# Kernel optimization log

Hardware: AMD Instinct MI355X
Metric: run time of the kernel (lower is better)

## Reference

```python
import jax, jax.numpy as jnp
import numpy as np

IMG = 224      # img_size
P = 16         # patch_size
C = 3          # in_chans
K = 100        # n_segments
COMPACT = 10.0 # slic compactness
ITERS = 10     # slic k-means iterations


def _resize_matrix(src, dst):
    # Linear antialiased resize is a linear map; materialize it by resizing identity.
    return jax.image.resize(jnp.eye(src, dtype=jnp.float32), (dst, src),
                            method='linear', antialias=True)


def _slic_labels(img_hwc):
    """Simplified SLIC: grid-initialized k-means in (color, compactness-scaled xy) space."""
    H, W = IMG, IMG
    S = float(np.sqrt(H * W / K))         # superpixel spacing
    ratio = COMPACT / S                   # spatial scaling (SLIC distance weighting)
    yy, xx = jnp.meshgrid(jnp.arange(H, dtype=jnp.float32),
                          jnp.arange(W, dtype=jnp.float32), indexing='ij')
    feat = jnp.concatenate([img_hwc, (yy * ratio)[..., None], (xx * ratio)[..., None]],
                           axis=-1).reshape(H * W, C + 2)  # [HW, 5]
    # grid init of K centers
    gh = int(np.ceil(np.sqrt(K)))
    gw = int(np.ceil(K / gh))
    cy = ((np.arange(gh) + 0.5) * H / gh).astype(np.int32)
    cx = ((np.arange(gw) + 0.5) * W / gw).astype(np.int32)
    idx = (cy[:, None] * W + cx[None, :]).reshape(-1)[:K]
    centers0 = feat[jnp.asarray(idx)]  # [K, 5]

    f2 = jnp.sum(feat * feat, axis=1, keepdims=True)  # [HW,1]

    def dists(centers):
        c2 = jnp.sum(centers * centers, axis=1)  # [K]
        return f2 + c2[None, :] - 2.0 * (feat @ centers.T)  # [HW,K]

    def body(i, centers):
        lbl = jnp.argmin(dists(centers), axis=1)              # [HW]
        oh = jax.nn.one_hot(lbl, K, dtype=feat.dtype)         # [HW,K]
        cnt = oh.sum(0)                                       # [K]
        new = (oh.T @ feat) / jnp.maximum(cnt, 1.0)[:, None]  # [K,5]
        return jnp.where((cnt > 0)[:, None], new, centers)

    centers = jax.lax.fori_loop(0, ITERS, body, centers0)
    return jnp.argmin(dists(centers), axis=1).reshape(H, W)


def _embed_one(img_chw, A):
    img = jnp.transpose(img_chw, (1, 2, 0))                     # [H,W,C]
    labels = jax.lax.stop_gradient(_slic_labels(img))           # [H,W] int
    masks = jax.nn.one_hot(labels, K, dtype=img.dtype, axis=0)  # [K,H,W]
    masked = masks[..., None] * img[None]                       # [K,H,W,C]
    tmp = jnp.einsum('ph,khwc->kpwc', A, masked)                # resize rows
    return jnp.einsum('qw,kpwc->kpqc', A, tmp)                  # [K,P,P,C]


def reference(x):
    B = x.shape[0]
    A = _resize_matrix(IMG, P)
    sp = jax.vmap(lambda im: _embed_one(im, A))(x)  # [B,K,P,P,C]
    # torch: view(B, K*C, P, P)  (raw row-major reinterpret), flatten(2), transpose(1,2)
    out = sp.reshape(B, K * C, P, P).reshape(B, K * C, P * P)
    return jnp.transpose(out, (0, 2, 1))  # [B, P*P, K*C]


def setup_inputs() -> dict:
    key = jax.random.key(0)
    x = jax.random.uniform(key, (8, C, IMG, IMG), dtype=jnp.float32)
    return {"x": x}
```

## Files before the change

kernel.cpp:

```cpp
#include <hip/hip_runtime.h>
#include <math.h>

#define IMGD 224
#define HW 50176
#define NK 100
#define NB 8
#define OUT_PER_B 76800
#define NCHUNK 131
#define MSTR 13


static __device__ __forceinline__ float ratio_f32() {
  return (float)(10.0 / sqrt(224.0 * 224.0 / 100.0));
}

static __device__ __forceinline__ float dist5s(float f0, float f1, float f2,
                                               float f3, float f4, float fsq,
                                               float c0, float c1, float c2,
                                               float c3, float c4, float q) {
  float dot = __fmul_rn(f0, c0);
  dot = __fmaf_rn(f1, c1, dot);
  dot = __fmaf_rn(f2, c2, dot);
  dot = __fmaf_rn(f3, c3, dot);
  dot = __fmaf_rn(f4, c4, dot);
  return __fsub_rn(__fadd_rn(fsq, q), __fmul_rn(2.0f, dot));
}

static __device__ __forceinline__ float fsq5(float f0, float f1, float f2,
                                             float f3, float f4) {
  float s = __fmul_rn(f0, f0);
  s = __fadd_rn(s, __fmul_rn(f1, f1));
  s = __fadd_rn(s, __fmul_rn(f2, f2));
  s = __fadd_rn(s, __fmul_rn(f3, f3));
  s = __fadd_rn(s, __fmul_rn(f4, f4));
  return s;
}

__global__ void __launch_bounds__(256, 4) iter_kernel(
    const float* __restrict__ x, float* __restrict__ centers,
    const float* __restrict__ c2g, float* __restrict__ partials, int flag,
    float* __restrict__ Ag) {
  __shared__ float4 ck4[NK];
  __shared__ float2 ck2[NK];
  __shared__ unsigned int maskS[2][NK * MSTR];
  __shared__ unsigned short ppkS[2][NK * MSTR];
  __shared__ float4 cval4[2][384];
  __shared__ float  cvalf[2][384];
  __shared__ int cntS[2][128];
  __shared__ int offxS[2][128];
  __shared__ int wtotS[2];
  __shared__ float ubpart[2][12][10];
  __shared__ float ubg[2][12];
  __shared__ unsigned int candm[2][12][4];
  __shared__ float ared[128];
  int bx = blockIdx.x, b = blockIdx.y;
  int tid = threadIdx.x;

  if (bx >= 66) {
    for (int rr = 0; rr < 2; ++rr) {
      int p = 2 * b + rr;
      float cp = (p + 0.5f) * 14.0f - 0.5f;
      if (tid < 128) {
        float xd0 = fabsf(cp - (float)tid) / 14.0f;
        float trip0 = fmaxf(0.0f, 1.0f - xd0);
        float trip1 = 0.0f;
        int t2 = tid + 128;
        if (t2 < IMGD) {
          float xd = fabsf(cp - (float)t2) / 14.0f;
          trip1 = fmaxf(0.0f, 1.0f - xd);
        }
        ared[tid] = trip0 + trip1;
      }
      __syncthreads();
      for (int s = 64; s > 0; s >>= 1) {
        if (tid < s) ared[tid] += ared[tid + s];
        __syncthreads();
      }
      float Zp = ared[0];
      __syncthreads();
      if (tid < IMGD) {
        float xd = fabsf(cp - (float)tid) / 14.0f;
        Ag[p * IMGD + tid] = fmaxf(0.0f, 1.0f - xd) / Zp;
      }
      __syncthreads();
    }
    return;
  }

  int half = tid >> 7;
  int lt = tid & 127;
  int c = 2 * bx + half;
  int start, len;
  if (c < NCHUNK) {
    start = (c < 129) ? c * 384 : 49536 + (c - 129) * 320;
    len   = (c < 129) ? 384 : 320;
  } else {
    start = 0; len = 0;
  }

  const float ratio = ratio_f32();
  const float* x0 = x + (size_t)b * 3 * HW;
  if (flag == 0) {
    if (tid < NK) {
      int gy = tid / 10, gx = tid - 10 * (tid / 10);
      int cy = (int)((gy + 0.5) * 224.0 / 10.0);
      int cx = (int)((gx + 0.5) * 224.0 / 10.0);
      int i = cy * IMGD + cx;
      float c0 = x0[i], c1 = x0[HW + i], c2 = x0[2 * HW + i];
      float c3 = __fmul_rn((float)cy, ratio);
      float c4 = __fmul_rn((float)cx, ratio);
      float s = __fmul_rn(c0, c0);
      s = __fadd_rn(s, __fmul_rn(c1, c1));
      s = __fadd_rn(s, __fmul_rn(c2, c2));
      s = __fadd_rn(s, __fmul_rn(c3, c3));
      s = __fadd_rn(s, __fmul_rn(c4, c4));
      ck4[tid] = make_float4(c0, c1, c2, c3);
      ck2[tid] = make_float2(c4, s);
      if (bx == 0) {
        float* oc = centers + ((size_t)b * NK + tid) * 5;
        oc[0] = c0; oc[1] = c1; oc[2] = c2; oc[3] = c3; oc[4] = c4;
      }
    }
  } else {
    const float* cb = centers + (size_t)b * NK * 5;
    const float* c2b = c2g + (size_t)b * NK;
    if (tid < NK) {
      ck4[tid] = make_float4(cb[tid*5+0], cb[tid*5+1], cb[tid*5+2], cb[tid*5+3]);
      ck2[tid] = make_float2(cb[tid*5+4], c2b[tid]);
    }
  }
  for (int t = lt; t < NK * MSTR; t += 128) maskS[half][t] = 0u;
  if (lt < 48) candm[half][lt >> 2][lt & 3] = 0u;

  float f0[3], f1[3], f2[3], f3[3], f4[3], fq[3];
  bool vld[3];
  for (int r = 0; r < 3; ++r) {
    int t = lt + r * 128;
    vld[r] = (t < len);
    int i = start + (vld[r] ? t : 0);
    int y = i / IMGD, xw = i - y * IMGD;
    f0[r] = x0[i]; f1[r] = x0[HW + i]; f2[r] = x0[2 * HW + i];
    f3[r] = __fmul_rn((float)y, ratio);
    f4[r] = __fmul_rn((float)xw, ratio);
    fq[r] = fsq5(f0[r], f1[r], f2[r], f3[r], f4[r]);
  }
  __syncthreads();

  if (lt < 120) {
    int g = lt / 10, kb = lt - 10 * g;
    int i0 = start + g * 32, i1 = i0 + 31;
    int ymin = i0 / IMGD, ymax = i1 / IMGD;
    int cmin = (ymin == ymax) ? (i0 - ymin * IMGD) : 0;
    int cmax = (ymin == ymax) ? (i1 - ymax * IMGD) : (IMGD - 1);
    float f3mn = __fmul_rn((float)ymin, ratio);
    float f3mx = __fmul_rn((float)ymax, ratio);
    float f4mn = __fmul_rn((float)cmin, ratio);
    float f4mx = __fmul_rn((float)cmax, ratio);
    float mn = 3.4e38f;
    for (int k = kb * 10; k < kb * 10 + 10; ++k) {
      float c3 = ck4[k].w, c4 = ck2[k].x;
      float dy = fmaxf(fabsf(c3 - f3mn), fabsf(c3 - f3mx));
      float dx = fmaxf(fabsf(c4 - f4mn), fabsf(c4 - f4mx));
      mn = fminf(mn, dy * dy + dx * dx + 3.0f);
    }
    ubpart[half][g][kb] = mn;
  }
  __syncthreads();
  if (lt < 12) {
    float mn = ubpart[half][lt][0];
    for (int j = 1; j < 10; ++j) mn = fminf(mn, ubpart[half][lt][j]);
    ubg[half][lt] = mn + 1.0f;
  }
  __syncthreads();
  if (lt < 120) {
    int g = lt / 10, kb = lt - 10 * g;
    int i0 = start + g * 32, i1 = i0 + 31;
    int ymin = i0 / IMGD, ymax = i1 / IMGD;
    int cmin = (ymin == ymax) ? (i0 - ymin * IMGD) : 0;
    int cmax = (ymin == ymax) ? (i1 - ymax * IMGD) : (IMGD - 1);
    float f3mn = __fmul_rn((float)ymin, ratio);
    float f3mx = __fmul_rn((float)ymax, ratio);
    float f4mn = __fmul_rn((float)cmin, ratio);
    float f4mx = __fmul_rn((float)cmax, ratio);
    float lim = ubg[half][g];
    for (int k = kb * 10; k < kb * 10 + 10; ++k) {
      float c3 = ck4[k].w, c4 = ck2[k].x;
      float dy = fmaxf(0.0f, fmaxf(f3mn - c3, c3 - f3mx));
      float dx = fmaxf(0.0f, fmaxf(f4mn - c4, c4 - f4mx));
      if (dy * dy + dx * dx <= lim)
        atomicOr(&candm[half][g][k >> 5], 1u << (k & 31));
    }
  }
  __syncthreads();

  float best[3]; int bk[3];
  for (int r = 0; r < 3; ++r) {
    best[r] = 3.4e38f; bk[r] = 0;
    int t = lt + r * 128;
    int g = (t < 384) ? (t >> 5) : 0;
    for (int w = 0; w < 4; ++w) {
      unsigned int m = candm[half][g][w];
      while (m) {
        int j = __ffs(m) - 1;
        m &= m - 1;
        int k = (w << 5) + j;
        float4 a4 = ck4[k];
        float2 a2 = ck2[k];
        float d = dist5s(f0[r], f1[r], f2[r], f3[r], f4[r], fq[r],
                         a4.x, a4.y, a4.z, a4.w, a2.x, a2.y);
        if (d < best[r]) { best[r] = d; bk[r] = k; }
      }
    }
  }
  for (int r = 0; r < 3; ++r) {
    int t = lt + r * 128;
    if (vld[r]) atomicOr(&maskS[half][bk[r] * MSTR + (t >> 5)], 1u << (t & 31));
  }
  __syncthreads();

  int myCnt = 0;
  if (lt < NK) {
    int s = 0;
    for (int g = 0; g < 12; ++g) {
      ppkS[half][lt * MSTR + g] = (unsigned short)s;
      s += __popc(maskS[half][lt * MSTR + g]);
    }
    myCnt = s;
  }
  cntS[half][lt] = myCnt;
  __syncthreads();

  int v = myCnt;
  for (int d = 1; d < 64; d <<= 1) {
    int u = __shfl_up(v, d, 64);
    if ((tid & 63) >= d) v += u;
  }
  if (lt == 63) wtotS[half] = v;
  __syncthreads();
  if (lt >= 64) v += wtotS[half];
  offxS[half][lt] = v;
  __syncthreads();

  for (int r = 0; r < 3; ++r) {
    int t = lt + r * 128;
    if (vld[r]) {
      int g = t >> 5, j = t & 31;
      unsigned int m = maskS[half][bk[r] * MSTR + g];
      int rank = ppkS[half][bk[r] * MSTR + g] + __popc(m & ((1u << j) - 1u));
      int pos = offxS[half][bk[r]] - cntS[half][bk[r]] + rank;
      cval4[half][pos] = make_float4(f0[r], f1[r], f2[r], f3[r]);
      cvalf[half][pos] = f4[r];
    }
  }
  __syncthreads();

  if (c < NCHUNK && lt < NK) {
    int n = cntS[half][lt];
    int base = offxS[half][lt] - n;
    float s0 = 0.f, s1 = 0.f, s2 = 0.f, s3 = 0.f, s4 = 0.f, s5 = 0.f;
    for (int m = 0; m < n; ++m) {
      float4 vv = cval4[half][base + m];
      float ww = cvalf[half][base + m];
      s0 = __fadd_rn(s0, vv.x);
      s1 = __fadd_rn(s1, vv.y);
      s2 = __fadd_rn(s2, vv.z);
      s3 = __fadd_rn(s3, vv.w);
      s4 = __fadd_rn(s4, ww);
      s5 += 1.0f;
    }
    float* pp = partials + ((size_t)(b * NK + lt) * 6) * NCHUNK + c;
    pp[0 * NCHUNK] = s0; pp[1 * NCHUNK] = s1; pp[2 * NCHUNK] = s2;
    pp[3 * NCHUNK] = s3; pp[4 * NCHUNK] = s4; pp[5 * NCHUNK] = s5;
  }
}

__global__ void __launch_bounds__(256) combine_update_kernel(
    float* __restrict__ centers, const float* __restrict__ partials,
    float* __restrict__ c2g) {
  __shared__ float st[8 * 6 * NCHUNK];
  __shared__ float sums[8][6];
  __shared__ float newc[8][5];
  int bb = blockIdx.x;
  int tid = threadIdx.x;
  const float* base = partials + (size_t)bb * 8 * 6 * NCHUNK;
  for (int t = tid; t < (8 * 6 * NCHUNK) / 4; t += 256)
    ((float4*)st)[t] = ((const float4*)base)[t];
  __syncthreads();
  if (tid < 48) {
    int row = tid / 6, comp = tid - 6 * (tid / 6);
    const float* rp = st + (row * 6 + comp) * NCHUNK;
    float s = rp[0];
    for (int c = 1; c < NCHUNK; ++c) s = __fadd_rn(s, rp[c]);
    sums[row][comp] = s;
  }
  __syncthreads();
  if (tid < 40) {
    int row = tid / 5, d = tid - 5 * (tid / 5);
    float cntv = sums[row][5];
    float* cc = centers + (size_t)(bb * 8 + row) * 5;
    float v;
    if (cntv > 0.0f) {
      float m = fmaxf(cntv, 1.0f);
      v = __fdiv_rn(sums[row][d], m);
      cc[d] = v;
    } else {
      v = cc[d];
    }
    newc[row][d] = v;
  }
  __syncthreads();
  if (tid < 8) {
    float t0 = __fmul_rn(newc[tid][0], newc[tid][0]);
    t0 = __fadd_rn(t0, __fmul_rn(newc[tid][1], newc[tid][1]));
    t0 = __fadd_rn(t0, __fmul_rn(newc[tid][2], newc[tid][2]));
    t0 = __fadd_rn(t0, __fmul_rn(newc[tid][3], newc[tid][3]));
    t0 = __fadd_rn(t0, __fmul_rn(newc[tid][4], newc[tid][4]));
    c2g[bb * 8 + tid] = t0;
  }
}

__global__ void __launch_bounds__(128, 4) label_kernel(
    const float* __restrict__ x, const float* __restrict__ centers,
    const float* __restrict__ c2g, unsigned char* __restrict__ labels) {
  __shared__ float4 ck4[NK];
  __shared__ float2 ck2[NK];
  __shared__ float ubpart[12][10];
  __shared__ float ubg[12];
  __shared__ unsigned int candm[12][4];
  int c = blockIdx.x, b = blockIdx.y;
  int tid = threadIdx.x;
  int start = (c < 129) ? c * 384 : 49536 + (c - 129) * 320;
  int len   = (c < 129) ? 384 : 320;

  const float ratio = ratio_f32();
  const float* x0 = x + (size_t)b * 3 * HW;
  const float* cb = centers + (size_t)b * NK * 5;
  const float* c2b = c2g + (size_t)b * NK;
  if (tid < NK) {
    ck4[tid] = make_float4(cb[tid*5+0], cb[tid*5+1], cb[tid*5+2], cb[tid*5+3]);
    ck2[tid] = make_float2(cb[tid*5+4], c2b[tid]);
  }
  if (tid < 48) candm[tid >> 2][tid & 3] = 0u;

  float f0[3], f1[3], f2[3], f3[3], f4[3], fq[3];
  int ii[3];
  bool vld[3];
  for (int r = 0; r < 3; ++r) {
    int t = tid + r * 128;
    vld[r] = (t < len);
    int i = start + (vld[r] ? t : 0);
    ii[r] = i;
    int y = i / IMGD, xw = i - y * IMGD;
    f0[r] = x0[i]; f1[r] = x0[HW + i]; f2[r] = x0[2 * HW + i];
    f3[r] = __fmul_rn((float)y, ratio);
    f4[r] = __fmul_rn((float)xw, ratio);
    fq[r] = fsq5(f0[r], f1[r], f2[r], f3[r], f4[r]);
  }
  __syncthreads();

  if (tid < 120) {
    int g = tid / 10, kb = tid - 10 * g;
    int i0 = start + g * 32, i1 = i0 + 31;
    int ymin = i0 / IMGD, ymax = i1 / IMGD;
    int cmin = (ymin == ymax) ? (i0 - ymin * IMGD) : 0;
    int cmax = (ymin == ymax) ? (i1 - ymax * IMGD) : (IMGD - 1);
    float f3mn = __fmul_rn((float)ymin, ratio);
    float f3mx = __fmul_rn((float)ymax, ratio);
    float f4mn = __fmul_rn((float)cmin, ratio);
    float f4mx = __fmul_rn((float)cmax, ratio);
    float mn = 3.4e38f;
    for (int k = kb * 10; k < kb * 10 + 10; ++k) {
      float c3 = ck4[k].w, c4 = ck2[k].x;
      float dy = fmaxf(fabsf(c3 - f3mn), fabsf(c3 - f3mx));
      float dx = fmaxf(fabsf(c4 - f4mn), fabsf(c4 - f4mx));
      mn = fminf(mn, dy * dy + dx * dx + 3.0f);
    }
    ubpart[g][kb] = mn;
  }
  __syncthreads();
  if (tid < 12) {
    float mn = ubpart[tid][0];
    for (int j = 1; j < 10; ++j) mn = fminf(mn, ubpart[tid][j]);
    ubg[tid] = mn + 1.0f;
  }
  __syncthreads();
  if (tid < 120) {
    int g = tid / 10, kb = tid - 10 * g;
    int i0 = start + g * 32, i1 = i0 + 31;
    int ymin = i0 / IMGD, ymax = i1 / IMGD;
    int cmin = (ymin == ymax) ? (i0 - ymin * IMGD) : 0;
    int cmax = (ymin == ymax) ? (i1 - ymax * IMGD) : (IMGD - 1);
    float f3mn = __fmul_rn((float)ymin, ratio);
    float f3mx = __fmul_rn((float)ymax, ratio);
    float f4mn = __fmul_rn((float)cmin, ratio);
    float f4mx = __fmul_rn((float)cmax, ratio);
    float lim = ubg[g];
    for (int k = kb * 10; k < kb * 10 + 10; ++k) {
      float c3 = ck4[k].w, c4 = ck2[k].x;
      float dy = fmaxf(0.0f, fmaxf(f3mn - c3, c3 - f3mx));
      float dx = fmaxf(0.0f, fmaxf(f4mn - c4, c4 - f4mx));
      if (dy * dy + dx * dx <= lim)
        atomicOr(&candm[g][k >> 5], 1u << (k & 31));
    }
  }
  __syncthreads();

  float best[3]; int bk[3];
  for (int r = 0; r < 3; ++r) {
    best[r] = 3.4e38f; bk[r] = 0;
    int t = tid + r * 128;
    int g = (t < 384) ? (t >> 5) : 0;
    for (int w = 0; w < 4; ++w) {
      unsigned int m = candm[g][w];
      while (m) {
        int j = __ffs(m) - 1;
        m &= m - 1;
        int k = (w << 5) + j;
        float4 a4 = ck4[k];
        float2 a2 = ck2[k];
        float d = dist5s(f0[r], f1[r], f2[r], f3[r], f4[r], fq[r],
                         a4.x, a4.y, a4.z, a4.w, a2.x, a2.y);
        if (d < best[r]) { best[r] = d; bk[r] = k; }
      }
    }
  }
  unsigned char* lb = labels + (size_t)b * HW;
  for (int r = 0; r < 3; ++r)
    if (vld[r]) lb[ii[r]] = (unsigned char)bk[r];
}

__global__ void __launch_bounds__(256) embed_kernel(
    const float* __restrict__ x, const unsigned char* __restrict__ labels,
    const float* __restrict__ Ag, float* __restrict__ out) {
  __shared__ float Apv[28];
  __shared__ float Aqw[4][28];
  __shared__ float sk[4][NK * 3];
  int b = blockIdx.y;
  int p = blockIdx.x >> 2;
  int qg = blockIdx.x & 3;
  int q0 = qg * 4;
  int tid = threadIdx.x;

  int h0 = max(0, 14 * p - 7), h1 = min(IMGD - 1, 14 * p + 20);
  int hl = h1 - h0 + 1;
  int w0q[4], w1q[4];
#pragma unroll
  for (int qi = 0; qi < 4; ++qi) {
    int q = q0 + qi;
    w0q[qi] = max(0, 14 * q - 7);
    w1q[qi] = min(IMGD - 1, 14 * q + 20);
  }
  int W0 = w0q[0], W1 = w1q[3];
  int WU = W1 - W0 + 1;

  if (tid < hl) Apv[tid] = Ag[p * IMGD + h0 + tid];
  {
    int t = tid - 64;
    if (t >= 0 && t < 112) {
      int qi = t / 28, dw = t - 28 * qi;
      if (dw <= w1q[qi] - w0q[qi])
        Aqw[qi][dw] = Ag[(q0 + qi) * IMGD + w0q[qi] + dw];
    }
  }
  for (int t = tid; t < 4 * NK * 3; t += 256)
    sk[t / (NK * 3)][t % (NK * 3)] = 0.0f;
  __syncthreads();

  const float* xb = x + (size_t)b * 3 * HW;
  const unsigned char* lb = labels + (size_t)b * HW;
  int n = hl * WU;
  for (int r = 0; r < 8; ++r) {
    int idx = tid + r * 256;
    if (idx >= n) break;
    int dh = idx / WU;
    int dcol = idx - dh * WU;
    int col = W0 + dcol;
    int i = (h0 + dh) * IMGD + col;
    float v0 = xb[i], v1 = xb[HW + i], v2 = xb[2 * HW + i];
    int k = lb[i];
    float ap = Apv[dh];
#pragma unroll
    for (int qi = 0; qi < 4; ++qi) {
      if (col >= w0q[qi] && col <= w1q[qi]) {
        float wgt = ap * Aqw[qi][col - w0q[qi]];
        atomicAdd(&sk[qi][k * 3 + 0], wgt * v0);
        atomicAdd(&sk[qi][k * 3 + 1], wgt * v1);
        atomicAdd(&sk[qi][k * 3 + 2], wgt * v2);
      }
    }
  }
  __syncthreads();

  float* outb = out + (size_t)b * OUT_PER_B;
  for (int t = tid; t < 4 * NK * 3; t += 256) {
    int qi = t / (NK * 3), t3 = t - qi * (NK * 3);
    int k = t3 / 3, cc = t3 - 3 * k;
    int base = p * 48 + (q0 + qi) * 3;
    int f = k * 768 + base + cc;
    outb[(f & 255) * 300 + (f >> 8)] = sk[qi][t3];
  }
}

extern "C" void kernel_launch(void* const* d_in, const int* in_sizes, int n_in,
                              void* d_out, int out_size, void* d_ws, size_t ws_size,
                              hipStream_t stream) {
  const float* x = (const float*)d_in[0];
  float* out = (float*)d_out;
  char* ws = (char*)d_ws;
  float* centers        = (float*)(ws + 16384);
  float* c2g            = (float*)(ws + 49152);
  float* Ag             = (float*)(ws + 65536);
  unsigned char* labels = (unsigned char*)(ws + 98304);
  float* partials       = (float*)(ws + 1703936);

  dim3 ig0(67, NB);
  dim3 ig(66, NB);
  iter_kernel<<<ig0, 256, 0, stream>>>(x, centers, c2g, partials, 0, Ag);
  combine_update_kernel<<<NB * NK / 8, 256, 0, stream>>>(centers, partials, c2g);
  for (int it = 1; it < 10; ++it) {
    iter_kernel<<<ig, 256, 0, stream>>>(x, centers, c2g, partials, 1, Ag);
    combine_update_kernel<<<NB * NK / 8, 256, 0, stream>>>(centers, partials, c2g);
  }
  label_kernel<<<dim3(NCHUNK, NB), 128, 0, stream>>>(x, centers, c2g, labels);
  dim3 egrid(64, NB);
  embed_kernel<<<egrid, 256, 0, stream>>>(x, labels, Ag, out);
}
```

Baseline: 292.1 us.

## Use wave-level shuffles and ballots for candidate pruning and prefix scan

```diff
diff --git a/kernel.cpp b/kernel.cpp
--- a/kernel.cpp
+++ b/kernel.cpp
@@ -42,15 +42,13 @@
     float* __restrict__ Ag) {
   __shared__ float4 ck4[NK];
   __shared__ float2 ck2[NK];
+  __shared__ float2 ckxy[NK];
   __shared__ unsigned int maskS[2][NK * MSTR];
   __shared__ unsigned short ppkS[2][NK * MSTR];
   __shared__ float4 cval4[2][384];
   __shared__ float  cvalf[2][384];
   __shared__ int cntS[2][128];
   __shared__ int offxS[2][128];
-  __shared__ int wtotS[2];
-  __shared__ float ubpart[2][12][10];
-  __shared__ float ubg[2][12];
   __shared__ unsigned int candm[2][12][4];
   __shared__ float ared[128];
   int bx = blockIdx.x, b = blockIdx.y;
@@ -116,6 +114,7 @@
       s = __fadd_rn(s, __fmul_rn(c4, c4));
       ck4[tid] = make_float4(c0, c1, c2, c3);
       ck2[tid] = make_float2(c4, s);
+      ckxy[tid] = make_float2(c3, c4);
       if (bx == 0) {
         float* oc = centers + ((size_t)b * NK + tid) * 5;
         oc[0] = c0; oc[1] = c1; oc[2] = c2; oc[3] = c3; oc[4] = c4;
@@ -127,10 +126,10 @@
     if (tid < NK) {
       ck4[tid] = make_float4(cb[tid*5+0], cb[tid*5+1], cb[tid*5+2], cb[tid*5+3]);
       ck2[tid] = make_float2(cb[tid*5+4], c2b[tid]);
+      ckxy[tid] = make_float2(cb[tid*5+3], cb[tid*5+4]);
     }
   }
   for (int t = lt; t < NK * MSTR; t += 128) maskS[half][t] = 0u;
-  if (lt < 48) candm[half][lt >> 2][lt & 3] = 0u;
 
   float f0[3], f1[3], f2[3], f3[3], f4[3], fq[3];
   bool vld[3];
@@ -146,49 +145,43 @@
   }
   __syncthreads();
 
-  if (lt < 120) {
-    int g = lt / 10, kb = lt - 10 * g;
-    int i0 = start + g * 32, i1 = i0 + 31;
-    int ymin = i0 / IMGD, ymax = i1 / IMGD;
-    int cmin = (ymin == ymax) ? (i0 - ymin * IMGD) : 0;
-    int cmax = (ymin == ymax) ? (i1 - ymax * IMGD) : (IMGD - 1);
-    float f3mn = __fmul_rn((float)ymin, ratio);
-    float f3mx = __fmul_rn((float)ymax, ratio);
-    float f4mn = __fmul_rn((float)cmin, ratio);
-    float f4mx = __fmul_rn((float)cmax, ratio);
-    float mn = 3.4e38f;
-    for (int k = kb * 10; k < kb * 10 + 10; ++k) {
-      float c3 = ck4[k].w, c4 = ck2[k].x;
-      float dy = fmaxf(fabsf(c3 - f3mn), fabsf(c3 - f3mx));
-      float dx = fmaxf(fabsf(c4 - f4mn), fabsf(c4 - f4mx));
-      mn = fminf(mn, dy * dy + dx * dx + 3.0f);
-    }
-    ubpart[half][g][kb] = mn;
-  }
-  __syncthreads();
-  if (lt < 12) {
-    float mn = ubpart[half][lt][0];
-    for (int j = 1; j < 10; ++j) mn = fminf(mn, ubpart[half][lt][j]);
-    ubg[half][lt] = mn + 1.0f;
-  }
-  __syncthreads();
-  if (lt < 120) {
-    int g = lt / 10, kb = lt - 10 * g;
-    int i0 = start + g * 32, i1 = i0 + 31;
-    int ymin = i0 / IMGD, ymax = i1 / IMGD;
-    int cmin = (ymin == ymax) ? (i0 - ymin * IMGD) : 0;
-    int cmax = (ymin == ymax) ? (i1 - ymax * IMGD) : (IMGD - 1);
-    float f3mn = __fmul_rn((float)ymin, ratio);
-    float f3mx = __fmul_rn((float)ymax, ratio);
-    float f4mn = __fmul_rn((float)cmin, ratio);
-    float f4mx = __fmul_rn((float)cmax, ratio);
-    float lim = ubg[half][g];
-    for (int k = kb * 10; k < kb * 10 + 10; ++k) {
-      float c3 = ck4[k].w, c4 = ck2[k].x;
-      float dy = fmaxf(0.0f, fmaxf(f3mn - c3, c3 - f3mx));
-      float dx = fmaxf(0.0f, fmaxf(f4mn - c4, c4 - f4mx));
-      if (dy * dy + dx * dx <= lim)
-        atomicOr(&candm[half][g][k >> 5], 1u << (k & 31));
+  {
+    int lane = tid & 63;
+    bool has2 = (lane < 36);
+    float2 cA = ckxy[lane];
+    float2 cB = ckxy[has2 ? (64 + lane) : 0];
+    int wv = lt >> 6;
+    for (int j = 0; j < 6; ++j) {
+      int g = wv * 6 + j;
+      int i0 = start + g * 32, i1 = i0 + 31;
+      int ymin = i0 / IMGD, ymax = i1 / IMGD;
+      int cmin = (ymin == ymax) ? (i0 - ymin * IMGD) : 0;
+      int cmax = (ymin == ymax) ? (i1 - ymax * IMGD) : (IMGD - 1);
+      float f3mn = __fmul_rn((float)ymin, ratio);
+      float f3mx = __fmul_rn((float)ymax, ratio);
+      float f4mn = __fmul_rn((float)cmin, ratio);
+      float f4mx = __fmul_rn((float)cmax, ratio);
+      float dyA = fmaxf(fabsf(cA.x - f3mn), fabsf(cA.x - f3mx));
+      float dxA = fmaxf(fabsf(cA.y - f4mn), fabsf(cA.y - f4mx));
+      float mA = dyA * dyA + dxA * dxA + 3.0f;
+      float dyB = fmaxf(fabsf(cB.x - f3mn), fabsf(cB.x - f3mx));
+      float dxB = fmaxf(fabsf(cB.y - f4mn), fabsf(cB.y - f4mx));
+      float mB = has2 ? (dyB * dyB + dxB * dxB + 3.0f) : 3.4e38f;
+      float mn = fminf(mA, mB);
+      for (int s = 1; s < 64; s <<= 1) mn = fminf(mn, __shfl_xor(mn, s, 64));
+      float lim = mn + 1.0f;
+      float eyA = fmaxf(0.0f, fmaxf(f3mn - cA.x, cA.x - f3mx));
+      float exA = fmaxf(0.0f, fmaxf(f4mn - cA.y, cA.y - f4mx));
+      unsigned long long b1 = __ballot(eyA * eyA + exA * exA <= lim);
+      float eyB = fmaxf(0.0f, fmaxf(f3mn - cB.x, cB.x - f3mx));
+      float exB = fmaxf(0.0f, fmaxf(f4mn - cB.y, cB.y - f4mx));
+      unsigned long long b2 = __ballot(has2 && (eyB * eyB + exB * exB <= lim));
+      if (lane == 0) {
+        candm[half][g][0] = (unsigned int)b1;
+        candm[half][g][1] = (unsigned int)(b1 >> 32);
+        candm[half][g][2] = (unsigned int)b2;
+        candm[half][g][3] = (unsigned int)(b2 >> 32);
+      }
     }
   }
   __syncthreads();
@@ -230,15 +223,17 @@
   cntS[half][lt] = myCnt;
   __syncthreads();
 
-  int v = myCnt;
-  for (int d = 1; d < 64; d <<= 1) {
-    int u = __shfl_up(v, d, 64);
-    if ((tid & 63) >= d) v += u;
-  }
-  if (lt == 63) wtotS[half] = v;
-  __syncthreads();
-  if (lt >= 64) v += wtotS[half];
-  offxS[half][lt] = v;
+  if ((lt >> 6) == 0) {
+    int a0 = cntS[half][2 * lt];
+    int a1 = cntS[half][2 * lt + 1];
+    int v = a0 + a1;
+    for (int d = 1; d < 64; d <<= 1) {
+      int u = __shfl_up(v, d, 64);
+      if (lt >= d) v += u;
+    }
+    offxS[half][2 * lt + 1] = v;
+    offxS[half][2 * lt]     = v - a1;
+  }
   __syncthreads();
 
   for (int r = 0; r < 3; ++r) {
@@ -324,8 +319,7 @@
     const float* __restrict__ c2g, unsigned char* __restrict__ labels) {
   __shared__ float4 ck4[NK];
   __shared__ float2 ck2[NK];
-  __shared__ float ubpart[12][10];
-  __shared__ float ubg[12];
+  __shared__ float2 ckxy[NK];
   __shared__ unsigned int candm[12][4];
   int c = blockIdx.x, b = blockIdx.y;
   int tid = threadIdx.x;
@@ -339,8 +333,8 @@
   if (tid < NK) {
     ck4[tid] = make_float4(cb[tid*5+0], cb[tid*5+1], cb[tid*5+2], cb[tid*5+3]);
     ck2[tid] = make_float2(cb[tid*5+4], c2b[tid]);
-  }
-  if (tid < 48) candm[tid >> 2][tid & 3] = 0u;
+    ckxy[tid] = make_float2(cb[tid*5+3], cb[tid*5+4]);
+  }
 
   float f0[3], f1[3], f2[3], f3[3], f4[3], fq[3];
   int ii[3];
@@ -358,49 +352,43 @@
   }
   __syncthreads();
 
-  if (tid < 120) {
-    int g = tid / 10, kb = tid - 10 * g;
-    int i0 = start + g * 32, i1 = i0 + 31;
-    int ymin = i0 / IMGD, ymax = i1 / IMGD;
-    int cmin = (ymin == ymax) ? (i0 - ymin * IMGD) : 0;
-    int cmax = (ymin == ymax) ? (i1 - ymax * IMGD) : (IMGD - 1);
-    float f3mn = __fmul_rn((float)ymin, ratio);
-    float f3mx = __fmul_rn((float)ymax, ratio);
-    float f4mn = __fmul_rn((float)cmin, ratio);
-    float f4mx = __fmul_rn((float)cmax, ratio);
-    float mn = 3.4e38f;
-    for (int k = kb * 10; k < kb * 10 + 10; ++k) {
-      float c3 = ck4[k].w, c4 = ck2[k].x;
-      float dy = fmaxf(fabsf(c3 - f3mn), fabsf(c3 - f3mx));
-      float dx = fmaxf(fabsf(c4 - f4mn), fabsf(c4 - f4mx));
-      mn = fminf(mn, dy * dy + dx * dx + 3.0f);
-    }
-    ubpart[g][kb] = mn;
-  }
-  __syncthreads();
-  if (tid < 12) {
-    float mn = ubpart[tid][0];
-    for (int j = 1; j < 10; ++j) mn = fminf(mn, ubpart[tid][j]);
-    ubg[tid] = mn + 1.0f;
-  }
-  __syncthreads();
-  if (tid < 120) {
-    int g = tid / 10, kb = tid - 10 * g;
-    int i0 = start + g * 32, i1 = i0 + 31;
-    int ymin = i0 / IMGD, ymax = i1 / IMGD;
-    int cmin = (ymin == ymax) ? (i0 - ymin * IMGD) : 0;
-    int cmax = (ymin == ymax) ? (i1 - ymax * IMGD) : (IMGD - 1);
-    float f3mn = __fmul_rn((float)ymin, ratio);
-    float f3mx = __fmul_rn((float)ymax, ratio);
-    float f4mn = __fmul_rn((float)cmin, ratio);
-    float f4mx = __fmul_rn((float)cmax, ratio);
-    float lim = ubg[g];
-    for (int k = kb * 10; k < kb * 10 + 10; ++k) {
-      float c3 = ck4[k].w, c4 = ck2[k].x;
-      float dy = fmaxf(0.0f, fmaxf(f3mn - c3, c3 - f3mx));
-      float dx = fmaxf(0.0f, fmaxf(f4mn - c4, c4 - f4mx));
-      if (dy * dy + dx * dx <= lim)
-        atomicOr(&candm[g][k >> 5], 1u << (k & 31));
+  {
+    int lane = tid & 63;
+    bool has2 = (lane < 36);
+    float2 cA = ckxy[lane];
+    float2 cB = ckxy[has2 ? (64 + lane) : 0];
+    int wv = tid >> 6;
+    for (int j = 0; j < 6; ++j) {
+      int g = wv * 6 + j;
+      int i0 = start + g * 32, i1 = i0 + 31;
+      int ymin = i0 / IMGD, ymax = i1 / IMGD;
+      int cmin = (ymin == ymax) ? (i0 - ymin * IMGD) : 0;
+      int cmax = (ymin == ymax) ? (i1 - ymax * IMGD) : (IMGD - 1);
+      float f3mn = __fmul_rn((float)ymin, ratio);
+      float f3mx = __fmul_rn((float)ymax, ratio);
+      float f4mn = __fmul_rn((float)cmin, ratio);
+      float f4mx = __fmul_rn((float)cmax, ratio);
+      float dyA = fmaxf(fabsf(cA.x - f3mn), fabsf(cA.x - f3mx));
+      float dxA = fmaxf(fabsf(cA.y - f4mn), fabsf(cA.y - f4mx));
+      float mA = dyA * dyA + dxA * dxA + 3.0f;
+      float dyB = fmaxf(fabsf(cB.x - f3mn), fabsf(cB.x - f3mx));
+      float dxB = fmaxf(fabsf(cB.y - f4mn), fabsf(cB.y - f4mx));
+      float mB = has2 ? (dyB * dyB + dxB * dxB + 3.0f) : 3.4e38f;
+      float mn = fminf(mA, mB);
+      for (int s = 1; s < 64; s <<= 1) mn = fminf(mn, __shfl_xor(mn, s, 64));
+      float lim = mn + 1.0f;
+      float eyA = fmaxf(0.0f, fmaxf(f3mn - cA.x, cA.x - f3mx));
+      float exA = fmaxf(0.0f, fmaxf(f4mn - cA.y, cA.y - f4mx));
+      unsigned long long b1 = __ballot(eyA * eyA + exA * exA <= lim);
+      float eyB = fmaxf(0.0f, fmaxf(f3mn - cB.x, cB.x - f3mx));
+      float exB = fmaxf(0.0f, fmaxf(f4mn - cB.y, cB.y - f4mx));
+      unsigned long long b2 = __ballot(has2 && (eyB * eyB + exB * exB <= lim));
+      if (lane == 0) {
+        candm[g][0] = (unsigned int)b1;
+        candm[g][1] = (unsigned int)(b1 >> 32);
+        candm[g][2] = (unsigned int)b2;
+        candm[g][3] = (unsigned int)(b2 >> 32);
+      }
     }
   }
   __syncthreads();
@@ -464,28 +452,40 @@
   }
   for (int t = tid; t < 4 * NK * 3; t += 256)
     sk[t / (NK * 3)][t % (NK * 3)] = 0.0f;
-  __syncthreads();
 
   const float* xb = x + (size_t)b * 3 * HW;
   const unsigned char* lb = labels + (size_t)b * HW;
   int n = hl * WU;
+  float pv0[8], pv1[8], pv2[8];
+  int pk[8], pdh[8], pdc[8];
+#pragma unroll
   for (int r = 0; r < 8; ++r) {
     int idx = tid + r * 256;
-    if (idx >= n) break;
-    int dh = idx / WU;
-    int dcol = idx - dh * WU;
-    int col = W0 + dcol;
-    int i = (h0 + dh) * IMGD + col;
-    float v0 = xb[i], v1 = xb[HW + i], v2 = xb[2 * HW + i];
-    int k = lb[i];
-    float ap = Apv[dh];
+    int idc = (idx < n) ? idx : 0;
+    int dh = idc / WU;
+    int dcol = idc - dh * WU;
+    int i = (h0 + dh) * IMGD + (W0 + dcol);
+    pv0[r] = xb[i]; pv1[r] = xb[HW + i]; pv2[r] = xb[2 * HW + i];
+    pk[r] = lb[i];
+    pdh[r] = dh; pdc[r] = dcol;
+  }
+  __syncthreads();
+
 #pragma unroll
-    for (int qi = 0; qi < 4; ++qi) {
-      if (col >= w0q[qi] && col <= w1q[qi]) {
-        float wgt = ap * Aqw[qi][col - w0q[qi]];
-        atomicAdd(&sk[qi][k * 3 + 0], wgt * v0);
-        atomicAdd(&sk[qi][k * 3 + 1], wgt * v1);
-        atomicAdd(&sk[qi][k * 3 + 2], wgt * v2);
+  for (int r = 0; r < 8; ++r) {
+    int idx = tid + r * 256;
+    if (idx < n) {
+      int col = W0 + pdc[r];
+      float ap = Apv[pdh[r]];
+      int k = pk[r];
+#pragma unroll
+      for (int qi = 0; qi < 4; ++qi) {
+        if (col >= w0q[qi] && col <= w1q[qi]) {
+          float wgt = ap * Aqw[qi][col - w0q[qi]];
+          atomicAdd(&sk[qi][k * 3 + 0], wgt * pv0[r]);
+          atomicAdd(&sk[qi][k * 3 + 1], wgt * pv1[r]);
+          atomicAdd(&sk[qi][k * 3 + 2], wgt * pv2[r]);
+        }
       }
     }
   }
```

New measurement: 297.9 us. About the same (+2.0%).
